# Kernel tuning notes

Measured on AMD Instinct MI355X. Metric: run time of the kernel, lower is better.

## Reference

```python
import jax, jax.numpy as jnp
import numpy as np

B, G, D = 256, 64, 20          # batch, genes per term, subsystem output dim
T3, T2, T1, T0 = 2048, 512, 128, 1  # terms per stratum, deepest first
FAN = 4                        # children per internal term (root gets all T1)
EPS = 1e-5                     # BatchNorm1d eps


def setup_inputs() -> dict:
    key = jax.random.key(0)
    ks = jax.random.split(key, 32)
    def genes(k, T):
        # binary gene perturbation states (column 3 of go_gene_strata_state)
        return (jax.random.uniform(k, (B, T, G)) < 0.5).astype(jnp.float32)
    def lin(kw, kb, T, din):
        # nn.init.uniform_(w, -0.001, 0.001) per DCellSubsystem
        W = jax.random.uniform(kw, (T, din, D), minval=-0.001, maxval=0.001)
        b = jax.random.uniform(kb, (T, D), minval=-0.001, maxval=0.001)
        return W, b
    in3, in2, in1, in0 = G, FAN * D + G, FAN * D + G, T1 * D + G
    W3, b3 = lin(ks[0], ks[1], T3, in3)
    W2, b2 = lin(ks[2], ks[3], T2, in2)
    W1, b1 = lin(ks[4], ks[5], T1, in1)
    W0, b0 = lin(ks[6], ks[7], T0, in0)
    ones = lambda T: jnp.ones((T, D), jnp.float32)
    zeros = lambda T: jnp.zeros((T, D), jnp.float32)
    hw0 = jax.random.normal(ks[8], (T0, D, 1)) * 0.1
    hb0 = jnp.zeros((T0, 1), jnp.float32)
    return {
        'genes3': genes(ks[9], T3), 'genes2': genes(ks[10], T2),
        'genes1': genes(ks[11], T1), 'genes0': genes(ks[12], T0),
        'W3': W3, 'b3': b3, 'g3': ones(T3), 'be3': zeros(T3),
        'W2': W2, 'b2': b2, 'g2': ones(T2), 'be2': zeros(T2),
        'W1': W1, 'b1': b1, 'g1': ones(T1), 'be1': zeros(T1),
        'W0': W0, 'b0': b0, 'g0': ones(T0), 'be0': zeros(T0),
        'hw0': hw0, 'hb0': hb0,
    }


def _subsystem(x, W, b, g, be):
    # Linear -> BatchNorm1d (training mode, batch stats over axis 0) -> Tanh
    z = jnp.einsum('bti,tio->bto', x, W) + b          # [B, T, D]
    mu = jnp.mean(z, axis=0)
    var = jnp.var(z, axis=0)                           # biased, as in torch BN
    zn = (z - mu) * jax.lax.rsqrt(var + EPS)
    return jnp.tanh(zn * g + be)


def reference(genes3, genes2, genes1, genes0,
              W3, b3, g3, be3, W2, b2, g2, be2,
              W1, b1, g1, be1, W0, b0, g0, be0, hw0, hb0):
    # stratum 3 (leaves): input is gene states only
    h3 = _subsystem(genes3, W3, b3, g3, be3)           # [B, T3, D]
    # stratum 2: concat FAN contiguous children + own gene states
    x2 = jnp.concatenate([h3.reshape(B, T2, FAN * D), genes2], axis=-1)
    h2 = _subsystem(x2, W2, b2, g2, be2)               # [B, T2, D]
    x1 = jnp.concatenate([h2.reshape(B, T1, FAN * D), genes1], axis=-1)
    h1 = _subsystem(x1, W1, b1, g1, be1)               # [B, T1, D]
    # root: all T1 children + root gene states
    x0 = jnp.concatenate([h1.reshape(B, T0, T1 * D), genes0], axis=-1)
    h0 = _subsystem(x0, W0, b0, g0, be0)               # [B, 1, D]
    pred = jnp.einsum('bto,toc->btc', h0, hw0) + hb0   # root linear head
    return pred.reshape(B, 1)
```

## Files before the change

kernel.cpp:

```cpp
#include <hip/hip_runtime.h>
#include <hip/hip_fp16.h>


#define DEV static __device__ __forceinline__

constexpr int B_  = 256, G_ = 64, D_ = 20;
constexpr int T3_ = 2048, T2_ = 512, T1_ = 128;
constexpr float EPS_ = 1e-5f;
constexpr int INM = 4 * D_ + G_;

constexpr size_t N_H3 = (size_t)T3_ * B_ * D_;
constexpr size_t N_H2 = (size_t)T2_ * B_ * D_;
constexpr size_t N_H1 = (size_t)B_ * T1_ * D_;
constexpr size_t OFF_H3B = 0;
constexpr size_t OFF_H2B = OFF_H3B + N_H3 * 2;
constexpr size_t OFF_H1B = OFF_H2B + N_H2 * 2;
constexpr size_t OFF_Z0B = OFF_H1B + N_H1 * 4;

DEV float fast_tanh(float x) {
    float e = __expf(2.0f * x);
    return fmaf(-2.0f, __builtin_amdgcn_rcpf(e + 1.0f), 1.0f);
}

template <int N>
DEV void bn_tanh(const float (&acc)[N], const float* gterm, const float* beterm,
                 int o0, int tid, float (&h)[N]) {
    __shared__ float sred[4][N], qred[4][N], Avec[N], Cvec[N];
    const int lane = tid & 63, wave = tid >> 6;
    float s[N], q[N];
#pragma unroll
    for (int o = 0; o < N; ++o) { s[o] = acc[o]; q[o] = acc[o] * acc[o]; }
#pragma unroll
    for (int off = 32; off; off >>= 1) {
#pragma unroll
        for (int o = 0; o < N; ++o) {
            s[o] += __shfl_xor(s[o], off, 64);
            q[o] += __shfl_xor(q[o], off, 64);
        }
    }
    if (lane == 0) {
#pragma unroll
        for (int o = 0; o < N; ++o) { sred[wave][o] = s[o]; qred[wave][o] = q[o]; }
    }
    __syncthreads();
    if (tid < N) {
        float S = sred[0][tid] + sred[1][tid] + sred[2][tid] + sred[3][tid];
        float Q = qred[0][tid] + qred[1][tid] + qred[2][tid] + qred[3][tid];
        float mu  = S * (1.0f / B_);
        float var = fmaxf(Q * (1.0f / B_) - mu * mu, 0.0f);
        float rstd = rsqrtf(var + EPS_);
        float A = rstd * gterm[o0 + tid];
        Avec[tid] = A;
        Cvec[tid] = beterm[o0 + tid] - mu * A;
    }
    __syncthreads();
#pragma unroll
    for (int o = 0; o < N; ++o) h[o] = fast_tanh(fmaf(acc[o], Avec[o], Cvec[o]));
}

__global__ __launch_bounds__(256, 4) void k_stage3(const float* __restrict__ genes,
                                                   const float* __restrict__ W,
                                                   const float* __restrict__ g,
                                                   const float* __restrict__ be,
                                                   __half* __restrict__ hout) {
    const int t = blockIdx.x, b = threadIdx.x;
    const float4* gp = (const float4*)(genes + ((size_t)b * T3_ + t) * G_);
    float4 xv[16];
#pragma unroll
    for (int v = 0; v < 16; ++v) xv[v] = gp[v];
    const float* Wt = W + (size_t)t * (G_ * D_);
    float acc[D_] = {};
#pragma unroll
    for (int v = 0; v < 16; ++v) {
        const float xs[4] = {xv[v].x, xv[v].y, xv[v].z, xv[v].w};
#pragma unroll
        for (int j = 0; j < 4; ++j) {
            const float* w = Wt + (4 * v + j) * D_;
#pragma unroll
            for (int o = 0; o < D_; ++o) acc[o] = fmaf(xs[j], w[o], acc[o]);
        }
    }
    float h[D_];
    bn_tanh<D_>(acc, g + (size_t)t * D_, be + (size_t)t * D_, 0, b, h);
    uint2* dst = (uint2*)(hout + ((size_t)t * B_ + b) * D_);
#pragma unroll
    for (int v = 0; v < 5; ++v) {
        union { __half2 h2[2]; uint2 u; } pk;
        pk.h2[0] = __floats2half2_rn(h[4 * v],     h[4 * v + 1]);
        pk.h2[1] = __floats2half2_rn(h[4 * v + 2], h[4 * v + 3]);
        dst[v] = pk.u;
    }
}

template <int T, int DCH, bool OUT_HALF_TERM_MAJOR>
__global__ __launch_bounds__(256, 4) void k_mid(const __half* __restrict__ hsrc,
                                                const float* __restrict__ genes,
                                                const float* __restrict__ W,
                                                const float* __restrict__ g,
                                                const float* __restrict__ be,
                                                void* __restrict__ hout_) {
    constexpr int NCH = D_ / DCH;
    const int t = blockIdx.x / NCH, o0 = (blockIdx.x % NCH) * DCH;
    const int b = threadIdx.x;
    const float* Wt = W + (size_t)t * (INM * D_) + o0;
    float acc[DCH] = {};
#pragma unroll
    for (int c = 0; c < 4; ++c) {
        const uint2* hp = (const uint2*)(hsrc + ((size_t)(4 * t + c) * B_ + b) * D_);
        float xc[D_];
#pragma unroll
        for (int v = 0; v < 5; ++v) {
            union { uint2 u; __half2 h2[2]; } pk;
            pk.u = hp[v];
            xc[4 * v]     = __low2float(pk.h2[0]);
            xc[4 * v + 1] = __high2float(pk.h2[0]);
            xc[4 * v + 2] = __low2float(pk.h2[1]);
            xc[4 * v + 3] = __high2float(pk.h2[1]);
        }
#pragma unroll
        for (int k = 0; k < D_; ++k) {
            const float* w = Wt + (c * D_ + k) * D_;
#pragma unroll
            for (int o = 0; o < DCH; ++o) acc[o] = fmaf(xc[k], w[o], acc[o]);
        }
    }
    const float4* gp = (const float4*)(genes + ((size_t)b * T + t) * G_);
#pragma unroll
    for (int v = 0; v < 16; ++v) {
        float4 f = gp[v];
        const float xs[4] = {f.x, f.y, f.z, f.w};
#pragma unroll
        for (int j = 0; j < 4; ++j) {
            const float* w = Wt + (4 * D_ + 4 * v + j) * D_;
#pragma unroll
            for (int o = 0; o < DCH; ++o) acc[o] = fmaf(xs[j], w[o], acc[o]);
        }
    }
    float h[DCH];
    bn_tanh<DCH>(acc, g + (size_t)t * D_, be + (size_t)t * D_, o0, b, h);
    if (OUT_HALF_TERM_MAJOR) {
        __half* hout = (__half*)hout_;
        uint* dst = (uint*)(hout + ((size_t)t * B_ + b) * D_ + o0);
#pragma unroll
        for (int v = 0; v < DCH / 2; ++v) {
            union { __half2 h2; uint u; } pk;
            pk.h2 = __floats2half2_rn(h[2 * v], h[2 * v + 1]);
            dst[v] = pk.u;
        }
    } else {
        float* dst = (float*)hout_ + ((size_t)b * T + t) * D_ + o0;
#pragma unroll
        for (int o = 0; o < DCH; ++o) dst[o] = h[o];
    }
}

__global__ __launch_bounds__(256, 4) void k_stage0a(const float* __restrict__ h1,
                                                    const float* __restrict__ genes0,
                                                    const float* __restrict__ W0,
                                                    float* __restrict__ z0) {
    const int b = blockIdx.x, tid = threadIdx.x;
    const float* x = h1 + (size_t)b * (T1_ * D_);
    float acc[D_] = {};
#pragma unroll
    for (int jj = 0; jj < (T1_ * D_) / 256; ++jj) {
        int k = tid + jj * 256;
        float xk = x[k];
        const float4* w = (const float4*)(W0 + (size_t)k * D_);
#pragma unroll
        for (int v = 0; v < D_ / 4; ++v) {
            float4 f = w[v];
            acc[4 * v + 0] = fmaf(xk, f.x, acc[4 * v + 0]);
            acc[4 * v + 1] = fmaf(xk, f.y, acc[4 * v + 1]);
            acc[4 * v + 2] = fmaf(xk, f.z, acc[4 * v + 2]);
            acc[4 * v + 3] = fmaf(xk, f.w, acc[4 * v + 3]);
        }
    }
    if (tid < G_) {
        float xk = genes0[(size_t)b * G_ + tid];
        const float4* w = (const float4*)(W0 + (size_t)(T1_ * D_ + tid) * D_);
#pragma unroll
        for (int v = 0; v < D_ / 4; ++v) {
            float4 f = w[v];
            acc[4 * v + 0] = fmaf(xk, f.x, acc[4 * v + 0]);
            acc[4 * v + 1] = fmaf(xk, f.y, acc[4 * v + 1]);
            acc[4 * v + 2] = fmaf(xk, f.z, acc[4 * v + 2]);
            acc[4 * v + 3] = fmaf(xk, f.w, acc[4 * v + 3]);
        }
    }
    __shared__ float sred[4][D_];
    const int lane = tid & 63, wave = tid >> 6;
#pragma unroll
    for (int off = 32; off; off >>= 1)
#pragma unroll
        for (int o = 0; o < D_; ++o) acc[o] += __shfl_xor(acc[o], off, 64);
    if (lane == 0)
#pragma unroll
        for (int o = 0; o < D_; ++o) sred[wave][o] = acc[o];
    __syncthreads();
    if (tid < D_)
        z0[(size_t)b * D_ + tid] = sred[0][tid] + sred[1][tid] + sred[2][tid] + sred[3][tid];
}

__global__ __launch_bounds__(256) void k_stage0b(const float* __restrict__ z0,
                                                 const float* __restrict__ g0,
                                                 const float* __restrict__ be0,
                                                 const float* __restrict__ hw0,
                                                 const float* __restrict__ hb0,
                                                 float* __restrict__ out) {
    const int tid = threadIdx.x;
    float acc[D_];
    const float4* zp = (const float4*)(z0 + (size_t)tid * D_);
#pragma unroll
    for (int v = 0; v < D_ / 4; ++v) {
        float4 f = zp[v];
        acc[4 * v + 0] = f.x; acc[4 * v + 1] = f.y;
        acc[4 * v + 2] = f.z; acc[4 * v + 3] = f.w;
    }
    float h[D_];
    bn_tanh<D_>(acc, g0, be0, 0, tid, h);
    __shared__ float hwv[D_ + 1];
    if (tid < D_) hwv[tid] = hw0[tid];
    if (tid == 0) hwv[D_] = hb0[0];
    __syncthreads();
    float pred = hwv[D_];
#pragma unroll
    for (int o = 0; o < D_; ++o) pred = fmaf(h[o], hwv[o], pred);
    out[tid] = pred;
}

extern "C" void kernel_launch(void* const* d_in, const int* in_sizes, int n_in,
                              void* d_out, int out_size, void* d_ws, size_t ws_size,
                              hipStream_t stream) {
    const float* genes3 = (const float*)d_in[0];
    const float* genes2 = (const float*)d_in[1];
    const float* genes1 = (const float*)d_in[2];
    const float* genes0 = (const float*)d_in[3];
    const float* W3  = (const float*)d_in[4];
    const float* g3  = (const float*)d_in[6];
    const float* be3 = (const float*)d_in[7];
    const float* W2  = (const float*)d_in[8];
    const float* g2  = (const float*)d_in[10];
    const float* be2 = (const float*)d_in[11];
    const float* W1  = (const float*)d_in[12];
    const float* g1  = (const float*)d_in[14];
    const float* be1 = (const float*)d_in[15];
    const float* W0  = (const float*)d_in[16];
    const float* g0  = (const float*)d_in[18];
    const float* be0 = (const float*)d_in[19];
    const float* hw0 = (const float*)d_in[20];
    const float* hb0 = (const float*)d_in[21];

    char* wsb = (char*)d_ws;
    __half* h3 = (__half*)(wsb + OFF_H3B);
    __half* h2 = (__half*)(wsb + OFF_H2B);
    float*  h1 = (float*)(wsb + OFF_H1B);
    float*  z0 = (float*)(wsb + OFF_Z0B);

    k_stage3<<<T3_, 256, 0, stream>>>(genes3, W3, g3, be3, h3);
    k_mid<T2_, 10, true ><<<T2_ * 2, 256, 0, stream>>>(h3, genes2, W2, g2, be2, h2);
    k_mid<T1_, 5,  false><<<T1_ * 4, 256, 0, stream>>>(h2, genes1, W1, g1, be1, h1);
    k_stage0a<<<B_, 256, 0, stream>>>(h1, genes0, W0, z0);
    k_stage0b<<<1, 256, 0, stream>>>(z0, g0, be0, hw0, hb0, (float*)d_out);
}
```

Baseline: 367.7 us.

## Stage genes and child activations through LDS with coalesced loads

Gene rows for each term are now loaded cooperatively with coalesced float4 reads, converted to half and stored in padded shared memory. Previously each thread read its own strided 256-byte row. The mid-stratum kernels also copy the four children's half activations into LDS in bulk, and they use wider output chunks (20 and 10) with launch bounds lowered to 2, so fewer blocks re-read the same inputs. Gene values go through fp16, which is exact for binary inputs. The cost is higher LDS use per block (about 33 KB plus 40 KB in k_mid), which limits occupancy.

```diff
diff --git a/kernel.cpp b/kernel.cpp
--- a/kernel.cpp
+++ b/kernel.cpp
@@ -17,9 +17,27 @@
 constexpr size_t OFF_H1B = OFF_H2B + N_H2 * 2;
 constexpr size_t OFF_Z0B = OFF_H1B + N_H1 * 4;
 
+constexpr int GSTRIDE_U = 33;
+
 DEV float fast_tanh(float x) {
     float e = __expf(2.0f * x);
     return fmaf(-2.0f, __builtin_amdgcn_rcpf(e + 1.0f), 1.0f);
+}
+
+DEV void stage_genes(const float* __restrict__ genes_t, size_t rowStrideF,
+                     uint* ldsg, int tid) {
+    const int e = tid & 15;
+    const int r0 = tid >> 4;
+#pragma unroll
+    for (int it = 0; it < 16; ++it) {
+        const int row = r0 + 16 * it;
+        float4 f = ((const float4*)(genes_t + (size_t)row * rowStrideF))[e];
+        union { __half2 h2; uint u; } p0, p1;
+        p0.h2 = __floats2half2_rn(f.x, f.y);
+        p1.h2 = __floats2half2_rn(f.z, f.w);
+        ldsg[GSTRIDE_U * row + 2 * e]     = p0.u;
+        ldsg[GSTRIDE_U * row + 2 * e + 1] = p1.u;
+    }
 }
 
 template <int N>
@@ -63,22 +81,23 @@
                                                    const float* __restrict__ g,
                                                    const float* __restrict__ be,
                                                    __half* __restrict__ hout) {
+    __shared__ uint ldsg[B_ * GSTRIDE_U];
     const int t = blockIdx.x, b = threadIdx.x;
-    const float4* gp = (const float4*)(genes + ((size_t)b * T3_ + t) * G_);
-    float4 xv[16];
-#pragma unroll
-    for (int v = 0; v < 16; ++v) xv[v] = gp[v];
+    stage_genes(genes + (size_t)t * G_, (size_t)T3_ * G_, ldsg, b);
+    __syncthreads();
     const float* Wt = W + (size_t)t * (G_ * D_);
     float acc[D_] = {};
 #pragma unroll
-    for (int v = 0; v < 16; ++v) {
-        const float xs[4] = {xv[v].x, xv[v].y, xv[v].z, xv[v].w};
-#pragma unroll
-        for (int j = 0; j < 4; ++j) {
-            const float* w = Wt + (4 * v + j) * D_;
-#pragma unroll
-            for (int o = 0; o < D_; ++o) acc[o] = fmaf(xs[j], w[o], acc[o]);
-        }
+    for (int g2 = 0; g2 < G_ / 2; ++g2) {
+        union { uint u; __half2 h2; } pk;
+        pk.u = ldsg[GSTRIDE_U * b + g2];
+        float x0 = __low2float(pk.h2), x1 = __high2float(pk.h2);
+        const float* w0 = Wt + (2 * g2) * D_;
+        const float* w1 = w0 + D_;
+#pragma unroll
+        for (int o = 0; o < D_; ++o) acc[o] = fmaf(x0, w0[o], acc[o]);
+#pragma unroll
+        for (int o = 0; o < D_; ++o) acc[o] = fmaf(x1, w1[o], acc[o]);
     }
     float h[D_];
     bn_tanh<D_>(acc, g + (size_t)t * D_, be + (size_t)t * D_, 0, b, h);
@@ -93,48 +112,53 @@
 }
 
 template <int T, int DCH, bool OUT_HALF_TERM_MAJOR>
-__global__ __launch_bounds__(256, 4) void k_mid(const __half* __restrict__ hsrc,
+__global__ __launch_bounds__(256, 2) void k_mid(const __half* __restrict__ hsrc,
                                                 const float* __restrict__ genes,
                                                 const float* __restrict__ W,
                                                 const float* __restrict__ g,
                                                 const float* __restrict__ be,
                                                 void* __restrict__ hout_) {
     constexpr int NCH = D_ / DCH;
+    constexpr int NCH4 = 4 * B_ * D_ / 8;
+    __shared__ uint ldsg[B_ * GSTRIDE_U];
+    __shared__ uint4 ldsh[NCH4];
     const int t = blockIdx.x / NCH, o0 = (blockIdx.x % NCH) * DCH;
     const int b = threadIdx.x;
+    const uint4* csrc = (const uint4*)(hsrc + (size_t)(4 * t) * B_ * D_);
+#pragma unroll
+    for (int it = 0; it < NCH4 / 256; ++it) ldsh[b + 256 * it] = csrc[b + 256 * it];
+    stage_genes(genes + (size_t)t * G_, (size_t)T * G_, ldsg, b);
+    __syncthreads();
+
     const float* Wt = W + (size_t)t * (INM * D_) + o0;
+    const __half* hc0 = (const __half*)ldsh;
     float acc[DCH] = {};
 #pragma unroll
     for (int c = 0; c < 4; ++c) {
-        const uint2* hp = (const uint2*)(hsrc + ((size_t)(4 * t + c) * B_ + b) * D_);
-        float xc[D_];
-#pragma unroll
-        for (int v = 0; v < 5; ++v) {
-            union { uint2 u; __half2 h2[2]; } pk;
-            pk.u = hp[v];
-            xc[4 * v]     = __low2float(pk.h2[0]);
-            xc[4 * v + 1] = __high2float(pk.h2[0]);
-            xc[4 * v + 2] = __low2float(pk.h2[1]);
-            xc[4 * v + 3] = __high2float(pk.h2[1]);
-        }
-#pragma unroll
-        for (int k = 0; k < D_; ++k) {
-            const float* w = Wt + (c * D_ + k) * D_;
-#pragma unroll
-            for (int o = 0; o < DCH; ++o) acc[o] = fmaf(xc[k], w[o], acc[o]);
-        }
-    }
-    const float4* gp = (const float4*)(genes + ((size_t)b * T + t) * G_);
-#pragma unroll
-    for (int v = 0; v < 16; ++v) {
-        float4 f = gp[v];
-        const float xs[4] = {f.x, f.y, f.z, f.w};
-#pragma unroll
-        for (int j = 0; j < 4; ++j) {
-            const float* w = Wt + (4 * D_ + 4 * v + j) * D_;
-#pragma unroll
-            for (int o = 0; o < DCH; ++o) acc[o] = fmaf(xs[j], w[o], acc[o]);
-        }
+        const __half* hc = hc0 + (size_t)(c * B_ + b) * D_;
+#pragma unroll
+        for (int v = 0; v < D_ / 2; ++v) {
+            __half2 hv = *(const __half2*)(hc + 2 * v);
+            float x0 = __low2float(hv), x1 = __high2float(hv);
+            const float* w0 = Wt + (c * D_ + 2 * v) * D_;
+            const float* w1 = w0 + D_;
+#pragma unroll
+            for (int o = 0; o < DCH; ++o) acc[o] = fmaf(x0, w0[o], acc[o]);
+#pragma unroll
+            for (int o = 0; o < DCH; ++o) acc[o] = fmaf(x1, w1[o], acc[o]);
+        }
+    }
+#pragma unroll
+    for (int g2 = 0; g2 < G_ / 2; ++g2) {
+        union { uint u; __half2 h2; } pk;
+        pk.u = ldsg[GSTRIDE_U * b + g2];
+        float x0 = __low2float(pk.h2), x1 = __high2float(pk.h2);
+        const float* w0 = Wt + (4 * D_ + 2 * g2) * D_;
+        const float* w1 = w0 + D_;
+#pragma unroll
+        for (int o = 0; o < DCH; ++o) acc[o] = fmaf(x0, w0[o], acc[o]);
+#pragma unroll
+        for (int o = 0; o < DCH; ++o) acc[o] = fmaf(x1, w1[o], acc[o]);
     }
     float h[DCH];
     bn_tanh<DCH>(acc, g + (size_t)t * D_, be + (size_t)t * D_, o0, b, h);
@@ -257,8 +281,8 @@
     float*  z0 = (float*)(wsb + OFF_Z0B);
 
     k_stage3<<<T3_, 256, 0, stream>>>(genes3, W3, g3, be3, h3);
-    k_mid<T2_, 10, true ><<<T2_ * 2, 256, 0, stream>>>(h3, genes2, W2, g2, be2, h2);
-    k_mid<T1_, 5,  false><<<T1_ * 4, 256, 0, stream>>>(h2, genes1, W1, g1, be1, h1);
+    k_mid<T2_, 20, true ><<<T2_, 256, 0, stream>>>(h3, genes2, W2, g2, be2, h2);
+    k_mid<T1_, 10, false><<<T1_ * 2, 256, 0, stream>>>(h2, genes1, W1, g1, be1, h1);
     k_stage0a<<<B_, 256, 0, stream>>>(h1, genes0, W0, z0);
     k_stage0b<<<1, 256, 0, stream>>>(z0, g0, be0, hw0, hb0, (float*)d_out);
 }
```

Result: slower. 399.3 us (+8.6%).
